# Performance work log

Measured on AMD Instinct MI355X. Metric: run time of the kernel, lower is better.

Reference implementation:

```python
import jax, jax.numpy as jnp
import numpy as np

P_SZ = 16      # patch size
N_PATCH = 196  # (224/16)^2
D = 768        # feat dim (= 3*16*16)
H = 3072       # mlp hidden
T = 8          # num task vectors
P_BLOCKS = 6   # param blocks: Wp, bp, W1, b1, W2, b2
META_H = 192   # max(768//4, T*P_BLOCKS)


def patchify(x):
    # x: [B,3,224,224] -> [B,196,768]
    B = x.shape[0]
    x = x.reshape(B, 3, 14, P_SZ, 14, P_SZ)
    x = x.transpose(0, 2, 4, 1, 3, 5)
    return x.reshape(B, N_PATCH, 3 * P_SZ * P_SZ)


def func0(params, xp):
    # surrogate linearized backbone on ONE sample's patches xp: [196,768] -> [768]
    Wp, bp, W1, b1, W2, b2 = params
    h = xp @ Wp + bp              # [196,768]
    f = h.mean(axis=0)            # [768]
    f = jax.nn.relu(f @ W1 + b1)  # [3072]
    return f @ W2 + b2            # [768]


def setup_inputs() -> dict:
    key = jax.random.key(0)
    ks = jax.random.split(key, 20)
    B = 32
    d = {}
    d['x'] = jax.random.normal(ks[0], (B, 3, 224, 224), dtype=jnp.float32)
    # base params0 (6 blocks)
    d['Wp'] = jax.random.normal(ks[1], (D, D), dtype=jnp.float32) * 0.02
    d['bp'] = jnp.zeros((D,), dtype=jnp.float32)
    d['W1'] = jax.random.normal(ks[2], (D, H), dtype=jnp.float32) * 0.02
    d['b1'] = jnp.zeros((H,), dtype=jnp.float32)
    d['W2'] = jax.random.normal(ks[3], (H, D), dtype=jnp.float32) * 0.02
    d['b2'] = jnp.zeros((D,), dtype=jnp.float32)
    # T stacked task-vector deltas, one per param block
    d['dWp'] = jax.random.normal(ks[4], (T, D, D), dtype=jnp.float32) * 0.01
    d['dbp'] = jax.random.normal(ks[5], (T, D), dtype=jnp.float32) * 0.01
    d['dW1'] = jax.random.normal(ks[6], (T, D, H), dtype=jnp.float32) * 0.01
    d['db1'] = jax.random.normal(ks[7], (T, H), dtype=jnp.float32) * 0.01
    d['dW2'] = jax.random.normal(ks[8], (T, H, D), dtype=jnp.float32) * 0.01
    d['db2'] = jax.random.normal(ks[9], (T, D), dtype=jnp.float32) * 0.01
    # MetaNet (Linear-ReLU-Linear), blockwise output T*P_BLOCKS
    d['mW1'] = jax.random.normal(ks[10], (D, META_H), dtype=jnp.float32) * 0.01
    d['mb1'] = jax.random.normal(ks[11], (META_H,), dtype=jnp.float32) * 0.01
    d['mW2'] = jax.random.normal(ks[12], (META_H, T * P_BLOCKS), dtype=jnp.float32) * 0.02
    d['mb2'] = jnp.zeros((T * P_BLOCKS,), dtype=jnp.float32)
    return d


def reference(x, Wp, bp, W1, b1, W2, b2,
              dWp, dbp, dW1, db1, dW2, db2,
              mW1, mb1, mW2, mb2):
    params0 = (Wp, bp, W1, b1, W2, b2)
    patches = patchify(x)                                  # [B,196,768]
    # base features (no grad in original)
    base_feat = jax.lax.stop_gradient(jax.vmap(lambda xp: func0(params0, xp))(patches))  # [B,768]
    # blockwise coefficients [B, T, P_BLOCKS]
    coefs = (jax.nn.relu(base_feat @ mW1 + mb1) @ mW2 + mb2).reshape(-1, T, P_BLOCKS)
    # batched weighted sum over task vectors, per parameter block
    dWp_b = jnp.einsum('bt,tij->bij', coefs[:, :, 0], dWp)
    dbp_b = jnp.einsum('bt,tj->bj',  coefs[:, :, 1], dbp)
    dW1_b = jnp.einsum('bt,tij->bij', coefs[:, :, 2], dW1)
    db1_b = jnp.einsum('bt,tj->bj',  coefs[:, :, 3], db1)
    dW2_b = jnp.einsum('bt,tij->bij', coefs[:, :, 4], dW2)
    db2_b = jnp.einsum('bt,tj->bj',  coefs[:, :, 5], db2)

    def single(xp, dp):
        out, dout = jax.jvp(lambda p: func0(p, xp), (params0,), (dp,))
        return out + dout

    outputs = jax.vmap(single)(patches, (dWp_b, dbp_b, dW1_b, db1_b, dW2_b, db2_b))
    return outputs  # [B,768]
```

## Files before the change

### kernel.cpp

```cpp
#include <hip/hip_runtime.h>


__global__ void patch_partial_k(const float* __restrict__ x, float* __restrict__ part) {
    int blk = blockIdx.x;
    int i  = blk % 14;
    int ch = (blk / 14) % 3;
    int b  = blk / 42;
    int t  = threadIdx.x;
    int py = t >> 4, px = t & 15;
    const float* xp = x + (((size_t)(b*3 + ch))*224 + (size_t)(i*16 + py))*224 + px;
    float s = 0.f;
#pragma unroll
    for (int j = 0; j < 14; ++j) s += xp[j*16];
    part[(size_t)blk*256 + t] = s;
}

__global__ void patch_reduce_k(const float* __restrict__ part, float* __restrict__ xbarT) {
    int idx = blockIdx.x*256 + threadIdx.x;
    int b = idx / 768;
    int c = idx % 768;
    int ch = c >> 8, t = c & 255;
    const float* p = part + ((size_t)(b*42 + ch*14))*256 + t;
    float s = 0.f;
#pragma unroll
    for (int i = 0; i < 14; ++i) s += p[i*256];
    xbarT[(size_t)c*32 + b] = s * (1.f/196.f);
}

#define PREFA(AR, K)                                                  \
    { AR[0] = *(const float4*)(ap7 + (K)*32);                         \
      AR[1] = *(const float4*)(ap7 + (K)*32 + 4); }

#define LOADB4(BUF)                                                   \
    { _Pragma("unroll")                                               \
      for (int u = 0; u < 4; ++u)                                     \
          BUF[u] = *(const float4*)(bp7 + (size_t)u*N);               \
      bp7 += (size_t)4*N; }

#define FMA4(AV, B4, base)                                            \
    acc[(base)+0] += (AV)*(B4).x; acc[(base)+1] += (AV)*(B4).y;       \
    acc[(base)+2] += (AV)*(B4).z; acc[(base)+3] += (AV)*(B4).w;

#define FMACK(AR, B4)                                                 \
    { FMA4(AR[0].x, B4, 0)  FMA4(AR[0].y, B4, 4)                      \
      FMA4(AR[0].z, B4, 8)  FMA4(AR[0].w, B4, 12)                     \
      FMA4(AR[1].x, B4, 16) FMA4(AR[1].y, B4, 20)                     \
      FMA4(AR[1].z, B4, 24) FMA4(AR[1].w, B4, 28) }

template<int N, int KB>
__global__ __launch_bounds__(256, 3) void gemm7_k(const float* __restrict__ AT,
                                                  const float* __restrict__ Bm,
                                                  float* __restrict__ P) {
    __shared__ float As[KB*32 + 32];
    const int tid  = threadIdx.x;
    const int lane = tid & 63;
    const int wave = tid >> 6;
    const int rg   = lane >> 4;
    const int cg   = lane & 15;
    const size_t kblk = (size_t)blockIdx.y * KB;

    {
        const float4* Ag = (const float4*)(AT + kblk*32);
        float4* As4 = (float4*)As;
        for (int i = tid; i < KB*8; i += 256) As4[i] = Ag[i];
    }

    const int col0 = blockIdx.x*256 + wave*64 + cg*4;
    const float* bp7 = Bm + kblk*N + col0;
    float4 bA[4], bB[4];
    LOADB4(bA)

    __syncthreads();
    const float* ap7 = As + rg*8;

    float acc[32];
#pragma unroll
    for (int m = 0; m < 32; ++m) acc[m] = 0.f;

    float4 a0[2], a1[2];
    PREFA(a0, 0)

#pragma unroll 1
    for (int kk = 0; kk + 8 <= KB; kk += 8) {
        LOADB4(bB)
        PREFA(a1, kk+1) FMACK(a0, bA[0])
        PREFA(a0, kk+2) FMACK(a1, bA[1])
        PREFA(a1, kk+3) FMACK(a0, bA[2])
        PREFA(a0, kk+4) FMACK(a1, bA[3])
        if (kk + 8 < KB) { LOADB4(bA) }
        PREFA(a1, kk+5) FMACK(a0, bB[0])
        PREFA(a0, kk+6) FMACK(a1, bB[1])
        PREFA(a1, kk+7) FMACK(a0, bB[2])
        PREFA(a0, kk+8) FMACK(a1, bB[3])
    }

    float* p0 = P + (size_t)blockIdx.y*((size_t)N*32) + (size_t)col0*32 + rg*8;
#pragma unroll
    for (int c = 0; c < 4; ++c) {
        *(float4*)(p0 + c*32)     = make_float4(acc[c], acc[4+c], acc[8+c], acc[12+c]);
        *(float4*)(p0 + c*32 + 4) = make_float4(acc[16+c], acc[20+c], acc[24+c], acc[28+c]);
    }
}

template<int Y>
__global__ void reduce_bias_k(const float* __restrict__ P, const float* __restrict__ bias,
                              float* __restrict__ out, int SZ) {
    int idx = blockIdx.x*256 + threadIdx.x;
    float s = bias[idx >> 5];
#pragma unroll 16
    for (int y = 0; y < Y; ++y) s += P[(size_t)y*SZ + idx];
    out[idx] = s;
}

template<int Y>
__global__ void reduce_zf_k(const float* __restrict__ P, const float* __restrict__ bias,
                            float* __restrict__ zT, float* __restrict__ fT) {
    int idx = blockIdx.x*256 + threadIdx.x;
    float s = bias[idx >> 5];
#pragma unroll 16
    for (int y = 0; y < Y; ++y) s += P[(size_t)y*98304 + idx];
    zT[idx] = s;
    fT[idx] = fmaxf(s, 0.f);
}

template<int Y>
__global__ void reduce_arr_k(const float* __restrict__ P, const float* __restrict__ init,
                             float* __restrict__ out, int SZ) {
    int idx = blockIdx.x*256 + threadIdx.x;
    float s = init[idx];
#pragma unroll 16
    for (int y = 0; y < Y; ++y) s += P[(size_t)y*SZ + idx];
    out[idx] = s;
}

template<int Y>
__global__ void reduce_mask_k(const float* __restrict__ P, const float* __restrict__ init,
                              const float* __restrict__ zT, float* __restrict__ dfT) {
    int idx = blockIdx.x*256 + threadIdx.x;
    float s = init[idx];
#pragma unroll 16
    for (int y = 0; y < Y; ++y) s += P[(size_t)y*98304 + idx];
    dfT[idx] = zT[idx] > 0.f ? s : 0.f;
}

template<int Y>
__global__ void reduce_out_k(const float* __restrict__ P, const float* __restrict__ init,
                             const float* __restrict__ baseT, float* __restrict__ out) {
    int idx = blockIdx.x*256 + threadIdx.x;
    float s = init[idx] + baseT[idx];
#pragma unroll 16
    for (int y = 0; y < Y; ++y) s += P[(size_t)y*24576 + idx];
    int n = idx >> 5, b = idx & 31;
    out[b*768 + n] = s;
}

__global__ void metanet1_k(const float* __restrict__ baseT, const float* __restrict__ mW1,
                           const float* __restrict__ mb1, float* __restrict__ v) {
    int b  = blockIdx.x;
    int jg = blockIdx.y;
    int jj = threadIdx.x & 31;
    int ks = threadIdx.x >> 5;
    int j  = jg*32 + jj;
    const float* wp = mW1 + (size_t)(ks*96)*192 + j;
    const float* xp = baseT + (size_t)(ks*96)*32 + b;
    float s = 0.f;
#pragma unroll 8
    for (int i = 0; i < 96; ++i) s += xp[i*32] * wp[i*192];
    __shared__ float red[256];
    red[threadIdx.x] = s;
    __syncthreads();
    if (threadIdx.x < 32) {
        float t = mb1[j];
#pragma unroll
        for (int k = 0; k < 8; ++k) t += red[k*32 + threadIdx.x];
        v[b*192 + jg*32 + threadIdx.x] = fmaxf(t, 0.f);
    }
}

__global__ void metanet2_k(const float* __restrict__ v, const float* __restrict__ mW2,
                           const float* __restrict__ mb2, float* __restrict__ coefs) {
    int b  = blockIdx.x;
    int o  = threadIdx.x & 63;
    int ks = threadIdx.x >> 6;
    float s = 0.f;
    if (o < 48) {
        const float* vp = v + b*192 + ks*48;
        const float* wp = mW2 + (size_t)(ks*48)*48 + o;
#pragma unroll 8
        for (int i = 0; i < 48; ++i) s += vp[i] * wp[i*48];
    }
    __shared__ float red[256];
    red[threadIdx.x] = s;
    __syncthreads();
    if (threadIdx.x < 48) {
        float t = mb2[threadIdx.x];
#pragma unroll
        for (int k = 0; k < 4; ++k) t += red[k*64 + threadIdx.x];
        coefs[b*48 + threadIdx.x] = t;
    }
}

__global__ void build_all_k(const float* __restrict__ coefs, const float* __restrict__ xbarT,
                            const float* __restrict__ f0T, const float* __restrict__ fT,
                            const float* __restrict__ dbp, const float* __restrict__ db1,
                            const float* __restrict__ db2,
                            float* __restrict__ G0T, float* __restrict__ G1T,
                            float* __restrict__ G2T, float* __restrict__ df0b,
                            float* __restrict__ dzb, float* __restrict__ doutb) {
    int idx = blockIdx.x*256 + threadIdx.x;
    int b = idx & 31;
    int r = idx >> 5;
    if (r < 6144) {
        int t = r / 768, i = r % 768;
        G0T[idx] = coefs[b*48 + t*6 + 0] * xbarT[(size_t)i*32 + b];
    } else if (r < 12288) {
        int rr = r - 6144;
        int t = rr / 768, i = rr % 768;
        G1T[(size_t)rr*32 + b] = coefs[b*48 + t*6 + 2] * f0T[(size_t)i*32 + b];
    } else if (r < 36864) {
        int rr = r - 12288;
        int t = rr / 3072, i = rr % 3072;
        G2T[(size_t)rr*32 + b] = coefs[b*48 + t*6 + 4] * fT[(size_t)i*32 + b];
    } else if (r < 37632) {
        int n = r - 36864;
        float s = 0.f;
#pragma unroll
        for (int t = 0; t < 8; ++t) s += coefs[b*48 + t*6 + 1] * dbp[t*768 + n];
        df0b[(size_t)n*32 + b] = s;
    } else if (r < 40704) {
        int n = r - 37632;
        float s = 0.f;
#pragma unroll
        for (int t = 0; t < 8; ++t) s += coefs[b*48 + t*6 + 3] * db1[t*3072 + n];
        dzb[(size_t)n*32 + b] = s;
    } else if (r < 41472) {
        int n = r - 40704;
        float s = 0.f;
#pragma unroll
        for (int t = 0; t < 8; ++t) s += coefs[b*48 + t*6 + 5] * db2[t*768 + n];
        doutb[(size_t)n*32 + b] = s;
    }
}

extern "C" void kernel_launch(void* const* d_in, const int* in_sizes, int n_in,
                              void* d_out, int out_size, void* d_ws, size_t ws_size,
                              hipStream_t stream) {
    const float* x   = (const float*)d_in[0];
    const float* Wp  = (const float*)d_in[1];
    const float* bp  = (const float*)d_in[2];
    const float* W1  = (const float*)d_in[3];
    const float* b1  = (const float*)d_in[4];
    const float* W2  = (const float*)d_in[5];
    const float* b2  = (const float*)d_in[6];
    const float* dWp = (const float*)d_in[7];
    const float* dbp = (const float*)d_in[8];
    const float* dW1 = (const float*)d_in[9];
    const float* db1 = (const float*)d_in[10];
    const float* dW2 = (const float*)d_in[11];
    const float* db2 = (const float*)d_in[12];
    const float* mW1 = (const float*)d_in[13];
    const float* mb1 = (const float*)d_in[14];
    const float* mW2 = (const float*)d_in[15];
    const float* mb2 = (const float*)d_in[16];
    float* out = (float*)d_out;

    float* ws    = (float*)d_ws;
    float* part  = ws;
    float* xbarT = part  + 344064;
    float* f0T   = xbarT + 24576;
    float* zT    = f0T   + 24576;
    float* fT    = zT    + 98304;
    float* baseT = fT    + 98304;
    float* coefs = baseT + 24576;
    float* G0T   = coefs + 1536;
    float* G1T   = G0T   + 196608;
    float* G2T   = G1T   + 196608;
    float* df0b  = G2T   + 786432;
    float* dzb   = df0b  + 24576;
    float* doutb = dzb   + 98304;
    float* dfT   = doutb + 24576;
    float* df0T  = dfT   + 98304;
    float* mv    = df0T  + 24576;
    float* A1 = mv + 6144;
    float* A2 = A1 + (size_t)80*98304;
    float* A3 = A2 + (size_t)320*24576;

    patch_partial_k<<<1344, 256, 0, stream>>>(x, part);
    patch_reduce_k<<<96, 256, 0, stream>>>(part, xbarT);

    gemm7_k<768, 48><<<dim3(3, 16), 256, 0, stream>>>(xbarT, Wp, A3);
    reduce_bias_k<16><<<96, 256, 0, stream>>>(A3, bp, f0T, 24576);
    gemm7_k<3072, 48><<<dim3(12, 16), 256, 0, stream>>>(f0T, W1, A1);
    reduce_zf_k<16><<<384, 256, 0, stream>>>(A1, b1, zT, fT);
    gemm7_k<768, 48><<<dim3(3, 64), 256, 0, stream>>>(fT, W2, A2);
    reduce_bias_k<64><<<96, 256, 0, stream>>>(A2, b2, baseT, 24576);

    metanet1_k<<<dim3(32, 6), 256, 0, stream>>>(baseT, mW1, mb1, mv);
    metanet2_k<<<32, 256, 0, stream>>>(mv, mW2, mb2, coefs);

    build_all_k<<<5184, 256, 0, stream>>>(coefs, xbarT, f0T, fT, dbp, db1, db2,
                                          G0T, G1T, G2T, df0b, dzb, doutb);

    gemm7_k<768, 48><<<dim3(3, 128), 256, 0, stream>>>(G0T, dWp, A3);
    reduce_arr_k<128><<<96, 256, 0, stream>>>(A3, df0b, df0T, 24576);
    gemm7_k<3072, 48><<<dim3(12, 16), 256, 0, stream>>>(df0T, W1, A1);
    gemm7_k<3072, 96><<<dim3(12, 64), 256, 0, stream>>>(G1T, dW1, A1 + (size_t)16*98304);
    reduce_mask_k<80><<<384, 256, 0, stream>>>(A1, dzb, zT, dfT);
    gemm7_k<768, 48><<<dim3(3, 64), 256, 0, stream>>>(dfT, W2, A2);
    gemm7_k<768, 96><<<dim3(3, 256), 256, 0, stream>>>(G2T, dW2, A2 + (size_t)64*24576);
    reduce_out_k<320><<<96, 256, 0, stream>>>(A2, doutb, baseT, out);
}
```

Measured before the change: 355.3 us.

## Stage B tiles into LDS via global_load_lds double buffering in skinny GEMM

Replaces the register-prefetched B-streaming GEMM with a version that copies 16-row slabs of the weight matrix straight into double-buffered LDS using the global_load_lds intrinsic. The small A operand is now read from global memory with wave-uniform addresses (scalar loads) instead of being staged in LDS. Occupancy hint is raised from 3 to 4 blocks. This aims to take the weight-streaming traffic off the VGPR path and overlap it better with compute, at the cost of a barrier and a full vmcnt wait per slab and a larger LDS footprint.

```diff
diff --git a/kernel.cpp b/kernel.cpp
--- a/kernel.cpp
+++ b/kernel.cpp
@@ -27,79 +27,67 @@
     xbarT[(size_t)c*32 + b] = s * (1.f/196.f);
 }
 
-#define PREFA(AR, K)                                                  \
-    { AR[0] = *(const float4*)(ap7 + (K)*32);                         \
-      AR[1] = *(const float4*)(ap7 + (K)*32 + 4); }
-
-#define LOADB4(BUF)                                                   \
-    { _Pragma("unroll")                                               \
-      for (int u = 0; u < 4; ++u)                                     \
-          BUF[u] = *(const float4*)(bp7 + (size_t)u*N);               \
-      bp7 += (size_t)4*N; }
-
-#define FMA4(AV, B4, base)                                            \
-    acc[(base)+0] += (AV)*(B4).x; acc[(base)+1] += (AV)*(B4).y;       \
-    acc[(base)+2] += (AV)*(B4).z; acc[(base)+3] += (AV)*(B4).w;
-
-#define FMACK(AR, B4)                                                 \
-    { FMA4(AR[0].x, B4, 0)  FMA4(AR[0].y, B4, 4)                      \
-      FMA4(AR[0].z, B4, 8)  FMA4(AR[0].w, B4, 12)                     \
-      FMA4(AR[1].x, B4, 16) FMA4(AR[1].y, B4, 20)                     \
-      FMA4(AR[1].z, B4, 24) FMA4(AR[1].w, B4, 28) }
-
 template<int N, int KB>
-__global__ __launch_bounds__(256, 3) void gemm7_k(const float* __restrict__ AT,
+__global__ __launch_bounds__(256, 4) void gemm8_k(const float* __restrict__ AT,
                                                   const float* __restrict__ Bm,
                                                   float* __restrict__ P) {
-    __shared__ float As[KB*32 + 32];
+    constexpr int NSLAB = KB / 16;
+    __shared__ float bbuf[2][16*256];
     const int tid  = threadIdx.x;
     const int lane = tid & 63;
-    const int wave = tid >> 6;
-    const int rg   = lane >> 4;
-    const int cg   = lane & 15;
+    const int wave = __builtin_amdgcn_readfirstlane(tid >> 6);
+    const int bx256 = blockIdx.x*256;
     const size_t kblk = (size_t)blockIdx.y * KB;
 
-    {
-        const float4* Ag = (const float4*)(AT + kblk*32);
-        float4* As4 = (float4*)As;
-        for (int i = tid; i < KB*8; i += 256) As4[i] = Ag[i];
-    }
-
-    const int col0 = blockIdx.x*256 + wave*64 + cg*4;
-    const float* bp7 = Bm + kblk*N + col0;
-    float4 bA[4], bB[4];
-    LOADB4(bA)
-
+#define STAGE8(PB, S)                                                          \
+    { _Pragma("unroll")                                                        \
+      for (int r = 0; r < 4; ++r) {                                            \
+        const float* gs = Bm + (kblk + (size_t)(S)*16 + wave*4 + r)*N          \
+                             + bx256 + lane*4;                                 \
+        __builtin_amdgcn_global_load_lds(                                      \
+            (const __attribute__((address_space(1))) void*)gs,                 \
+            (__attribute__((address_space(3))) void*)&bbuf[PB][(wave*4+r)*256],\
+            16, 0, 0);                                                         \
+      } }
+
+    STAGE8(0, 0)
+
+    float acc[32];
+#pragma unroll
+    for (int m = 0; m < 32; ++m) acc[m] = 0.f;
+
+    asm volatile("s_waitcnt vmcnt(0)" ::: "memory");
     __syncthreads();
-    const float* ap7 = As + rg*8;
-
-    float acc[32];
-#pragma unroll
-    for (int m = 0; m < 32; ++m) acc[m] = 0.f;
-
-    float4 a0[2], a1[2];
-    PREFA(a0, 0)
 
 #pragma unroll 1
-    for (int kk = 0; kk + 8 <= KB; kk += 8) {
-        LOADB4(bB)
-        PREFA(a1, kk+1) FMACK(a0, bA[0])
-        PREFA(a0, kk+2) FMACK(a1, bA[1])
-        PREFA(a1, kk+3) FMACK(a0, bA[2])
-        PREFA(a0, kk+4) FMACK(a1, bA[3])
-        if (kk + 8 < KB) { LOADB4(bA) }
-        PREFA(a1, kk+5) FMACK(a0, bB[0])
-        PREFA(a0, kk+6) FMACK(a1, bB[1])
-        PREFA(a1, kk+7) FMACK(a0, bB[2])
-        PREFA(a0, kk+8) FMACK(a1, bB[3])
-    }
-
-    float* p0 = P + (size_t)blockIdx.y*((size_t)N*32) + (size_t)col0*32 + rg*8;
+    for (int s = 0; s < NSLAB; ++s) {
+        if (s + 1 < NSLAB) STAGE8((s+1)&1, s+1)
+        const float* bs = &bbuf[s&1][0];
+        const float* ar = AT + (kblk + (size_t)s*16)*32 + wave*8;
+#pragma unroll
+        for (int kk = 0; kk < 16; ++kk) {
+            float4 bv = *(const float4*)(bs + kk*256 + lane*4);
+#pragma unroll
+            for (int r = 0; r < 8; ++r) {
+                float av = ar[kk*32 + r];
+                acc[r*4+0] += av * bv.x;
+                acc[r*4+1] += av * bv.y;
+                acc[r*4+2] += av * bv.z;
+                acc[r*4+3] += av * bv.w;
+            }
+        }
+        asm volatile("s_waitcnt vmcnt(0)" ::: "memory");
+        __syncthreads();
+    }
+
+    float* p0 = P + (size_t)blockIdx.y*((size_t)N*32)
+                  + (size_t)(bx256 + lane*4)*32 + wave*8;
 #pragma unroll
     for (int c = 0; c < 4; ++c) {
-        *(float4*)(p0 + c*32)     = make_float4(acc[c], acc[4+c], acc[8+c], acc[12+c]);
-        *(float4*)(p0 + c*32 + 4) = make_float4(acc[16+c], acc[20+c], acc[24+c], acc[28+c]);
-    }
+        *(float4*)(p0 + (size_t)c*32)     = make_float4(acc[c],    acc[4+c],  acc[8+c],  acc[12+c]);
+        *(float4*)(p0 + (size_t)c*32 + 4) = make_float4(acc[16+c], acc[20+c], acc[24+c], acc[28+c]);
+    }
+#undef STAGE8
 }
 
 template<int Y>
@@ -288,11 +276,11 @@
     patch_partial_k<<<1344, 256, 0, stream>>>(x, part);
     patch_reduce_k<<<96, 256, 0, stream>>>(part, xbarT);
 
-    gemm7_k<768, 48><<<dim3(3, 16), 256, 0, stream>>>(xbarT, Wp, A3);
+    gemm8_k<768, 48><<<dim3(3, 16), 256, 0, stream>>>(xbarT, Wp, A3);
     reduce_bias_k<16><<<96, 256, 0, stream>>>(A3, bp, f0T, 24576);
-    gemm7_k<3072, 48><<<dim3(12, 16), 256, 0, stream>>>(f0T, W1, A1);
+    gemm8_k<3072, 48><<<dim3(12, 16), 256, 0, stream>>>(f0T, W1, A1);
     reduce_zf_k<16><<<384, 256, 0, stream>>>(A1, b1, zT, fT);
-    gemm7_k<768, 48><<<dim3(3, 64), 256, 0, stream>>>(fT, W2, A2);
+    gemm8_k<768, 48><<<dim3(3, 64), 256, 0, stream>>>(fT, W2, A2);
     reduce_bias_k<64><<<96, 256, 0, stream>>>(A2, b2, baseT, 24576);
 
     metanet1_k<<<dim3(32, 6), 256, 0, stream>>>(baseT, mW1, mb1, mv);
@@ -301,12 +289,12 @@
     build_all_k<<<5184, 256, 0, stream>>>(coefs, xbarT, f0T, fT, dbp, db1, db2,
                                           G0T, G1T, G2T, df0b, dzb, doutb);
 
-    gemm7_k<768, 48><<<dim3(3, 128), 256, 0, stream>>>(G0T, dWp, A3);
+    gemm8_k<768, 48><<<dim3(3, 128), 256, 0, stream>>>(G0T, dWp, A3);
     reduce_arr_k<128><<<96, 256, 0, stream>>>(A3, df0b, df0T, 24576);
-    gemm7_k<3072, 48><<<dim3(12, 16), 256, 0, stream>>>(df0T, W1, A1);
-    gemm7_k<3072, 96><<<dim3(12, 64), 256, 0, stream>>>(G1T, dW1, A1 + (size_t)16*98304);
+    gemm8_k<3072, 48><<<dim3(12, 16), 256, 0, stream>>>(df0T, W1, A1);
+    gemm8_k<3072, 96><<<dim3(12, 64), 256, 0, stream>>>(G1T, dW1, A1 + (size_t)16*98304);
     reduce_mask_k<80><<<384, 256, 0, stream>>>(A1, dzb, zT, dfT);
-    gemm7_k<768, 48><<<dim3(3, 64), 256, 0, stream>>>(dfT, W2, A2);
-    gemm7_k<768, 96><<<dim3(3, 256), 256, 0, stream>>>(G2T, dW2, A2 + (size_t)64*24576);
+    gemm8_k<768, 48><<<dim3(3, 64), 256, 0, stream>>>(dfT, W2, A2);
+    gemm8_k<768, 96><<<dim3(3, 256), 256, 0, stream>>>(G2T, dW2, A2 + (size_t)64*24576);
     reduce_out_k<320><<<96, 256, 0, stream>>>(A2, doutb, baseT, out);
 }
```

Result: slower. 379.0 us (+6.7%).
